# Kernel tuning notes

Hardware: AMD Instinct MI355X
Metric: run time of the kernel (lower is better)

## Reference

```python
import jax, jax.numpy as jnp
import numpy as np

B, T, S, SYM, FFT = 256, 4, 2, 14, 128   # batch, num_tx, streams_per_tx, ofdm symbols, fft size
NSC, GUARD = 108, 10                      # effective subcarriers, guard offset
L = SYM * NSC                             # 1512, de-mash matrix dimension


def setup_inputs() -> dict:
    key = jax.random.key(0)
    k1, k2, k3, k4 = jax.random.split(key, 4)
    scale = 1.0 / np.sqrt(L).astype(np.float32)  # keep C roughly unitary-scaled
    return {
        "x_real": jax.random.normal(k1, (B, T, S, SYM, FFT), jnp.float32),
        "x_imag": jax.random.normal(k2, (B, T, S, SYM, FFT), jnp.float32),
        "C_real": jax.random.normal(k3, (L, L), jnp.float32) * scale,
        "C_imag": jax.random.normal(k4, (L, L), jnp.float32) * scale,
        "sc_ind": jnp.arange(NSC, dtype=jnp.int32) + GUARD,  # effective subcarrier indices
    }


def reference(x_real, x_imag, C_real, C_imag, sc_ind):
    # Complex RG and de-mash matrix
    x = jax.lax.complex(x_real, x_imag)           # [B,T,S,SYM,FFT] complex64
    C = jax.lax.complex(C_real, C_imag)           # [L,L] complex64

    # gather effective subcarriers along last axis
    y = jnp.take(x, sc_ind, axis=-1)              # [B,T,S,SYM,NSC]
    b, t, s, sym, nsc = y.shape

    # flatten_last_dims(y, 2) and multiply from right by C^H (adjoint=True)
    yf = y.reshape(b, t, s, sym * nsc)            # [B,T,S,L]
    yf = jnp.einsum('btsl,ml->btsm', yf, jnp.conj(C))  # y @ C^H
    y = yf.reshape(b, t, s, sym, nsc)             # [B,T,S,SYM,NSC]

    # scatter back into the full grid (equivalent to the transpose/scatter_nd/transpose chain,
    # since sc_ind is unique and the scatter is along the subcarrier axis)
    out = jnp.zeros(x.shape, x.dtype).at[..., sc_ind].set(y)

    # return real/imag stacked so the output is a single float32 array
    return jnp.stack([out.real, out.imag], axis=0)  # [2,B,T,S,SYM,FFT]
```

## Files before the change

### kernel.cpp

```cpp
#include <hip/hip_runtime.h>
#include <cstdint>
#include <cstddef>


typedef _Float16 half_t;
typedef half_t half8 __attribute__((ext_vector_type(8)));
typedef float floatx4 __attribute__((ext_vector_type(4)));

#define M_DIM 2048
#define N_DIM 3072
#define K_DIM 3072
#define LDIM 1512
#define NSC 108
#define SYMS 14
#define FFT 128
#define ROWLEN (SYMS * FFT)

#define BM 64
#define BN 128
#define BK 64

#define PA_BLOCKS 3072
#define PW_BLOCKS 4608
#define PG_BLOCKS 4480

typedef __attribute__((address_space(3))) uint32_t lds_u32_t;
typedef const __attribute__((address_space(1))) uint32_t glob_u32_t;

__device__ __forceinline__ void gl2lds16(const void* g, void* l) {
    __builtin_amdgcn_global_load_lds((glob_u32_t*)g, (lds_u32_t*)l, 16, 0, 0);
}

__global__ __launch_bounds__(256) void prep_all(
    const float* __restrict__ xr, const float* __restrict__ xi,
    const float* __restrict__ Cr, const float* __restrict__ Ci,
    const int* __restrict__ sc,
    half_t* __restrict__ A, half_t* __restrict__ W, float* __restrict__ out)
{
    const int b = blockIdx.x;
    const int t = threadIdx.x;

    if (b < PA_BLOCKS) {
        int idx = b * 256 + t;
        int row = idx / 384;
        int k0 = (idx - row * 384) * 8;
        half_t v[8];
        const float* src = nullptr;
        int kb = k0;
        if (k0 < LDIM)            { src = xr; }
        else if (k0 < 2 * LDIM)   { src = xi; kb = k0 - LDIM; }
        if (src) {
            const float* rowp = src + (size_t)row * ROWLEN;
#pragma unroll
            for (int e = 0; e < 8; ++e) {
                int k = kb + e;
                int sym = k / NSC;
                int j = k - sym * NSC;
                v[e] = (half_t)rowp[sym * FFT + sc[j]];
            }
        } else {
#pragma unroll
            for (int e = 0; e < 8; ++e) v[e] = (half_t)0.0f;
        }
        *(half8*)(A + (size_t)row * K_DIM + k0) = *(half8*)v;
    } else if (b < PA_BLOCKS + PW_BLOCKS) {
        int idx = (b - PA_BLOCKS) * 256 + t;
        int n = idx / 384;
        int k0 = (idx - n * 384) * 8;
        half_t v[8];
        const float* src = nullptr;
        float sgn = 1.0f;
        int nn = n, kb = k0;
        if (n < LDIM) {
            if (k0 < LDIM)            { src = Cr; }
            else if (k0 < 2 * LDIM)   { src = Ci; kb = k0 - LDIM; }
        } else if (n < 2 * LDIM) {
            nn = n - LDIM;
            if (k0 < LDIM)            { src = Ci; sgn = -1.0f; }
            else if (k0 < 2 * LDIM)   { src = Cr; kb = k0 - LDIM; }
        }
        if (src) {
            const float* rowp = src + (size_t)nn * LDIM + kb;
#pragma unroll
            for (int e = 0; e < 8; ++e) v[e] = (half_t)(sgn * rowp[e]);
        } else {
#pragma unroll
            for (int e = 0; e < 8; ++e) v[e] = (half_t)0.0f;
        }
        *(half8*)(W + (size_t)n * K_DIM + k0) = *(half8*)v;
    } else {
        int idx = (b - PA_BLOCKS - PW_BLOCKS) * 256 + t;
        int c20 = idx % 20;
        int rest = idx / 20;
        int sym = rest % 14;
        int rowri = rest / 14;
        int col = (c20 < 10) ? c20 : (NSC + c20);
        out[(size_t)rowri * ROWLEN + sym * FFT + col] = 0.0f;
    }
}

__global__ __launch_bounds__(256) void gemm_scatter(
    const half_t* __restrict__ A,
    const half_t* __restrict__ W,
    const int* __restrict__ sc,
    float* __restrict__ out)
{
    __shared__ __align__(16) half_t As[BM * BK];
    __shared__ __align__(16) half_t Bs[BN * BK];

    const int t = threadIdx.x;
    const int bn = blockIdx.x;
    const int bm = blockIdx.y;
    const int lane = t & 63;
    const int wn = (t >> 6) * 32;

    floatx4 acc[4][2] = {};

    const half_t* gAp[2];
    const half_t* gBp[4];
    half_t* lAp[2];
    half_t* lBp[4];
#pragma unroll
    for (int r = 0; r < 2; ++r) {
        int c = r * 256 + t;
        int row = c >> 3, slot = c & 7;
        int g = slot ^ (row & 7);
        gAp[r] = A + (size_t)(bm * BM + row) * K_DIM + g * 8;
        lAp[r] = As + c * 8;
    }
#pragma unroll
    for (int r = 0; r < 4; ++r) {
        int c = r * 256 + t;
        int row = c >> 3, slot = c & 7;
        int g = slot ^ (row & 7);
        gBp[r] = W + (size_t)(bn * BN + row) * K_DIM + g * 8;
        lBp[r] = Bs + c * 8;
    }

    const int fr = lane & 15;
    const int cr = lane >> 4;
    const int slot0 = (cr) ^ (fr & 7);
    const int slot1 = (4 + cr) ^ (fr & 7);

    for (int kb = 0; kb < K_DIM / BK; ++kb) {
        __syncthreads();
        gl2lds16(gAp[0], lAp[0]);
        gl2lds16(gAp[1], lAp[1]);
        gl2lds16(gBp[0], lBp[0]);
        gl2lds16(gBp[1], lBp[1]);
        gl2lds16(gBp[2], lBp[2]);
        gl2lds16(gBp[3], lBp[3]);
        gAp[0] += BK; gAp[1] += BK;
        gBp[0] += BK; gBp[1] += BK; gBp[2] += BK; gBp[3] += BK;
        __syncthreads();

        half8 af[2][4], bf[2][2];
#pragma unroll
        for (int i = 0; i < 4; ++i) {
            int rbase = (i * 16 + fr) * BK;
            af[0][i] = *(const half8*)&As[rbase + slot0 * 8];
            af[1][i] = *(const half8*)&As[rbase + slot1 * 8];
        }
#pragma unroll
        for (int j = 0; j < 2; ++j) {
            int rbase = (wn + j * 16 + fr) * BK;
            bf[0][j] = *(const half8*)&Bs[rbase + slot0 * 8];
            bf[1][j] = *(const half8*)&Bs[rbase + slot1 * 8];
        }
#pragma unroll
        for (int s = 0; s < 2; ++s)
#pragma unroll
            for (int i = 0; i < 4; ++i)
#pragma unroll
                for (int j = 0; j < 2; ++j)
                    acc[i][j] = __builtin_amdgcn_mfma_f32_16x16x32_f16(
                        af[s][i], bf[s][j], acc[i][j], 0, 0, 0);
    }

    const int col_base = bn * BN + wn + (lane & 15);
    const int row_base = bm * BM + ((lane >> 4) * 4);
#pragma unroll
    for (int j = 0; j < 2; ++j) {
        int n = col_base + j * 16;
        if (n >= 2 * LDIM) continue;
        int ri = (n >= LDIM) ? 1 : 0;
        int nn = n - ri * LDIM;
        int sym = nn / NSC;
        int jj = nn - sym * NSC;
        size_t colOff = (size_t)ri * (M_DIM * ROWLEN) + sym * FFT + sc[jj];
#pragma unroll
        for (int i = 0; i < 4; ++i) {
            int row0 = row_base + i * 16;
#pragma unroll
            for (int r = 0; r < 4; ++r) {
                out[colOff + (size_t)(row0 + r) * ROWLEN] = acc[i][j][r];
            }
        }
    }
}

extern "C" void kernel_launch(void* const* d_in, const int* in_sizes, int n_in,
                              void* d_out, int out_size, void* d_ws, size_t ws_size,
                              hipStream_t stream) {
    const float* xr = (const float*)d_in[0];
    const float* xi = (const float*)d_in[1];
    const float* Cr = (const float*)d_in[2];
    const float* Ci = (const float*)d_in[3];
    const int* sc   = (const int*)d_in[4];
    float* out = (float*)d_out;

    half_t* Ah = (half_t*)d_ws;
    half_t* Wh = (half_t*)((char*)d_ws + (size_t)M_DIM * K_DIM * 2);

    prep_all<<<PA_BLOCKS + PW_BLOCKS + PG_BLOCKS, 256, 0, stream>>>(
        xr, xi, Cr, Ci, sc, Ah, Wh, out);

    dim3 grid(N_DIM / BN, M_DIM / BM);
    gemm_scatter<<<grid, 256, 0, stream>>>(Ah, Wh, sc, out);
}
```

Measured before the change: 160.9 us.

## Double-buffer LDS tiles in GEMM and simplify gather index math

The GEMM main loop now uses two LDS buffers for A and W tiles. It prefetches the next K-tile with direct global-to-LDS loads while MFMAs consume the current tile, which removes one barrier per iteration and is meant to hide global load latency. The prep kernel also replaces the per-element divide when gathering subcarriers with an incrementing symbol/subcarrier counter. Doubling LDS per block may reduce occupancy. The overlap also depends on the compiler not inserting a full vmcnt wait before the LDS reads.

```diff
diff --git a/kernel.cpp b/kernel.cpp
--- a/kernel.cpp
+++ b/kernel.cpp
@@ -19,6 +19,7 @@
 #define BM 64
 #define BN 128
 #define BK 64
+#define NITER (K_DIM / BK)
 
 #define PA_BLOCKS 3072
 #define PW_BLOCKS 4608
@@ -51,12 +52,12 @@
         else if (k0 < 2 * LDIM)   { src = xi; kb = k0 - LDIM; }
         if (src) {
             const float* rowp = src + (size_t)row * ROWLEN;
+            int sym = kb / NSC;
+            int j = kb - sym * NSC;
 #pragma unroll
             for (int e = 0; e < 8; ++e) {
-                int k = kb + e;
-                int sym = k / NSC;
-                int j = k - sym * NSC;
                 v[e] = (half_t)rowp[sym * FFT + sc[j]];
+                if (++j == NSC) { j = 0; ++sym; }
             }
         } else {
 #pragma unroll
@@ -105,8 +106,8 @@
     const int* __restrict__ sc,
     float* __restrict__ out)
 {
-    __shared__ __align__(16) half_t As[BM * BK];
-    __shared__ __align__(16) half_t Bs[BN * BK];
+    __shared__ __align__(16) half_t As[2][BM * BK];
+    __shared__ __align__(16) half_t Bs[2][BN * BK];
 
     const int t = threadIdx.x;
     const int bn = blockIdx.x;
@@ -118,15 +119,14 @@
 
     const half_t* gAp[2];
     const half_t* gBp[4];
-    half_t* lAp[2];
-    half_t* lBp[4];
+    int ofsA[2], ofsB[4];
 #pragma unroll
     for (int r = 0; r < 2; ++r) {
         int c = r * 256 + t;
         int row = c >> 3, slot = c & 7;
         int g = slot ^ (row & 7);
         gAp[r] = A + (size_t)(bm * BM + row) * K_DIM + g * 8;
-        lAp[r] = As + c * 8;
+        ofsA[r] = c * 8;
     }
 #pragma unroll
     for (int r = 0; r < 4; ++r) {
@@ -134,7 +134,7 @@
         int row = c >> 3, slot = c & 7;
         int g = slot ^ (row & 7);
         gBp[r] = W + (size_t)(bn * BN + row) * K_DIM + g * 8;
-        lBp[r] = Bs + c * 8;
+        ofsB[r] = c * 8;
     }
 
     const int fr = lane & 15;
@@ -142,30 +142,42 @@
     const int slot0 = (cr) ^ (fr & 7);
     const int slot1 = (4 + cr) ^ (fr & 7);
 
-    for (int kb = 0; kb < K_DIM / BK; ++kb) {
+    gl2lds16(gAp[0], &As[0][ofsA[0]]);
+    gl2lds16(gAp[1], &As[0][ofsA[1]]);
+    gl2lds16(gBp[0], &Bs[0][ofsB[0]]);
+    gl2lds16(gBp[1], &Bs[0][ofsB[1]]);
+    gl2lds16(gBp[2], &Bs[0][ofsB[2]]);
+    gl2lds16(gBp[3], &Bs[0][ofsB[3]]);
+    gAp[0] += BK; gAp[1] += BK;
+    gBp[0] += BK; gBp[1] += BK; gBp[2] += BK; gBp[3] += BK;
+
+    for (int kb = 0; kb < NITER; ++kb) {
+        const int cur = kb & 1;
         __syncthreads();
-        gl2lds16(gAp[0], lAp[0]);
-        gl2lds16(gAp[1], lAp[1]);
-        gl2lds16(gBp[0], lBp[0]);
-        gl2lds16(gBp[1], lBp[1]);
-        gl2lds16(gBp[2], lBp[2]);
-        gl2lds16(gBp[3], lBp[3]);
-        gAp[0] += BK; gAp[1] += BK;
-        gBp[0] += BK; gBp[1] += BK; gBp[2] += BK; gBp[3] += BK;
-        __syncthreads();
+        if (kb + 1 < NITER) {
+            const int nxt = cur ^ 1;
+            gl2lds16(gAp[0], &As[nxt][ofsA[0]]);
+            gl2lds16(gAp[1], &As[nxt][ofsA[1]]);
+            gl2lds16(gBp[0], &Bs[nxt][ofsB[0]]);
+            gl2lds16(gBp[1], &Bs[nxt][ofsB[1]]);
+            gl2lds16(gBp[2], &Bs[nxt][ofsB[2]]);
+            gl2lds16(gBp[3], &Bs[nxt][ofsB[3]]);
+            gAp[0] += BK; gAp[1] += BK;
+            gBp[0] += BK; gBp[1] += BK; gBp[2] += BK; gBp[3] += BK;
+        }
 
         half8 af[2][4], bf[2][2];
 #pragma unroll
         for (int i = 0; i < 4; ++i) {
             int rbase = (i * 16 + fr) * BK;
-            af[0][i] = *(const half8*)&As[rbase + slot0 * 8];
-            af[1][i] = *(const half8*)&As[rbase + slot1 * 8];
+            af[0][i] = *(const half8*)&As[cur][rbase + slot0 * 8];
+            af[1][i] = *(const half8*)&As[cur][rbase + slot1 * 8];
         }
 #pragma unroll
         for (int j = 0; j < 2; ++j) {
             int rbase = (wn + j * 16 + fr) * BK;
-            bf[0][j] = *(const half8*)&Bs[rbase + slot0 * 8];
-            bf[1][j] = *(const half8*)&Bs[rbase + slot1 * 8];
+            bf[0][j] = *(const half8*)&Bs[cur][rbase + slot0 * 8];
+            bf[1][j] = *(const half8*)&Bs[cur][rbase + slot1 * 8];
         }
 #pragma unroll
         for (int s = 0; s < 2; ++s)
```

New measurement: 167.7 us. +4.2%, slower.

## Enlarge GEMM block tile to 128x128 with 2x2 wave layout

Applied to the files above, without the earlier changes.

Doubles the M tile of the GEMM block from 64 to 128 and arranges the four waves in a 2x2 grid, so each wave computes a 64x64 sub-tile with 16 accumulators instead of 8. This raises MFMA work per LDS fragment load and halves redundant global traffic for the W operand. The grid shrinks to 384 blocks and register and LDS use per block go up, which may cut occupancy. It also simplifies the index math in the A-prep gather by stepping the symbol and subcarrier counters instead of dividing per element.

```diff
diff --git a/kernel.cpp b/kernel.cpp
--- a/kernel.cpp
+++ b/kernel.cpp
@@ -16,9 +16,10 @@
 #define FFT 128
 #define ROWLEN (SYMS * FFT)
 
-#define BM 64
+#define BM 128
 #define BN 128
 #define BK 64
+#define NITER (K_DIM / BK)
 
 #define PA_BLOCKS 3072
 #define PW_BLOCKS 4608
@@ -51,12 +52,12 @@
         else if (k0 < 2 * LDIM)   { src = xi; kb = k0 - LDIM; }
         if (src) {
             const float* rowp = src + (size_t)row * ROWLEN;
+            int sym = kb / NSC;
+            int j = kb - sym * NSC;
 #pragma unroll
             for (int e = 0; e < 8; ++e) {
-                int k = kb + e;
-                int sym = k / NSC;
-                int j = k - sym * NSC;
                 v[e] = (half_t)rowp[sym * FFT + sc[j]];
+                if (++j == NSC) { j = 0; ++sym; }
             }
         } else {
 #pragma unroll
@@ -112,27 +113,23 @@
     const int bn = blockIdx.x;
     const int bm = blockIdx.y;
     const int lane = t & 63;
-    const int wn = (t >> 6) * 32;
-
-    floatx4 acc[4][2] = {};
-
-    const half_t* gAp[2];
+    const int wave = t >> 6;
+    const int wm = (wave & 1) * 64;
+    const int wn = (wave >> 1) * 64;
+
+    floatx4 acc[4][4] = {};
+
+    const half_t* gAp[4];
     const half_t* gBp[4];
-    half_t* lAp[2];
+    half_t* lAp[4];
     half_t* lBp[4];
 #pragma unroll
-    for (int r = 0; r < 2; ++r) {
+    for (int r = 0; r < 4; ++r) {
         int c = r * 256 + t;
         int row = c >> 3, slot = c & 7;
         int g = slot ^ (row & 7);
         gAp[r] = A + (size_t)(bm * BM + row) * K_DIM + g * 8;
         lAp[r] = As + c * 8;
-    }
-#pragma unroll
-    for (int r = 0; r < 4; ++r) {
-        int c = r * 256 + t;
-        int row = c >> 3, slot = c & 7;
-        int g = slot ^ (row & 7);
         gBp[r] = W + (size_t)(bn * BN + row) * K_DIM + g * 8;
         lBp[r] = Bs + c * 8;
     }
@@ -142,27 +139,26 @@
     const int slot0 = (cr) ^ (fr & 7);
     const int slot1 = (4 + cr) ^ (fr & 7);
 
-    for (int kb = 0; kb < K_DIM / BK; ++kb) {
+    for (int kb = 0; kb < NITER; ++kb) {
         __syncthreads();
-        gl2lds16(gAp[0], lAp[0]);
-        gl2lds16(gAp[1], lAp[1]);
-        gl2lds16(gBp[0], lBp[0]);
-        gl2lds16(gBp[1], lBp[1]);
-        gl2lds16(gBp[2], lBp[2]);
-        gl2lds16(gBp[3], lBp[3]);
-        gAp[0] += BK; gAp[1] += BK;
-        gBp[0] += BK; gBp[1] += BK; gBp[2] += BK; gBp[3] += BK;
+#pragma unroll
+        for (int r = 0; r < 4; ++r) {
+            gl2lds16(gAp[r], lAp[r]);
+            gl2lds16(gBp[r], lBp[r]);
+            gAp[r] += BK;
+            gBp[r] += BK;
+        }
         __syncthreads();
 
-        half8 af[2][4], bf[2][2];
+        half8 af[2][4], bf[2][4];
 #pragma unroll
         for (int i = 0; i < 4; ++i) {
-            int rbase = (i * 16 + fr) * BK;
+            int rbase = (wm + i * 16 + fr) * BK;
             af[0][i] = *(const half8*)&As[rbase + slot0 * 8];
             af[1][i] = *(const half8*)&As[rbase + slot1 * 8];
         }
 #pragma unroll
-        for (int j = 0; j < 2; ++j) {
+        for (int j = 0; j < 4; ++j) {
             int rbase = (wn + j * 16 + fr) * BK;
             bf[0][j] = *(const half8*)&Bs[rbase + slot0 * 8];
             bf[1][j] = *(const half8*)&Bs[rbase + slot1 * 8];
@@ -172,15 +168,15 @@
 #pragma unroll
             for (int i = 0; i < 4; ++i)
 #pragma unroll
-                for (int j = 0; j < 2; ++j)
+                for (int j = 0; j < 4; ++j)
                     acc[i][j] = __builtin_amdgcn_mfma_f32_16x16x32_f16(
                         af[s][i], bf[s][j], acc[i][j], 0, 0, 0);
     }
 
     const int col_base = bn * BN + wn + (lane & 15);
-    const int row_base = bm * BM + ((lane >> 4) * 4);
-#pragma unroll
-    for (int j = 0; j < 2; ++j) {
+    const int row_base = bm * BM + wm + ((lane >> 4) * 4);
+#pragma unroll
+    for (int j = 0; j < 4; ++j) {
         int n = col_base + j * 16;
         if (n >= 2 * LDIM) continue;
         int ri = (n >= LDIM) ? 1 : 0;
```

Measured after the change: 162.7 us. No clear change (+1.2%).
